# Optimization experiments

Hardware: AMD Instinct MI355X
Metric: run time of the kernel (lower is better)

## Reference

```python
import jax, jax.numpy as jnp
import numpy as np

N_V, N_Q, K, C, FF, OUT, H = 100000, 20000, 48, 128, 256, 128, 8
EPS = 1e-5

def _bn(x, g, b):
    # BatchNorm1d in training mode: biased batch stats over the voxel dim
    m = jnp.mean(x, axis=0)
    v = jnp.var(x, axis=0)
    return (x - m) * jax.lax.rsqrt(v + EPS) * g + b

def setup_inputs():
    key = jax.random.key(0)
    ks = jax.random.split(key, 12)
    s = 0.05
    return {
        "voxel_features": jax.random.normal(ks[0], (N_V, C), jnp.float32),
        "voxel_coords": jax.random.uniform(ks[1], (N_V, 3), jnp.float32) * 70.0,
        "query_coords": jax.random.uniform(ks[2], (N_Q, 3), jnp.float32) * 70.0,
        "wq3": jax.random.normal(ks[3], (3, C), jnp.float32) * s,
        "bq3": jnp.zeros((C,), jnp.float32),
        "wk3": jax.random.normal(ks[4], (3, C), jnp.float32) * s,
        "bk3": jnp.zeros((C,), jnp.float32),
        "in_proj_w": jax.random.normal(ks[5], (3 * C, C), jnp.float32) * s,
        "in_proj_b": jnp.zeros((3 * C,), jnp.float32),
        "out_w": jax.random.normal(ks[6], (C, C), jnp.float32) * s,
        "out_b": jnp.zeros((C,), jnp.float32),
        "w1": jax.random.normal(ks[7], (C, FF), jnp.float32) * s,
        "b1": jnp.zeros((FF,), jnp.float32),
        "w2": jax.random.normal(ks[8], (FF, C), jnp.float32) * s,
        "b2": jnp.zeros((C,), jnp.float32),
        "g1": jnp.ones((C,), jnp.float32),
        "be1": jnp.zeros((C,), jnp.float32),
        "w_out": jax.random.normal(ks[9], (C, OUT), jnp.float32) * s,
        "b_out": jnp.zeros((OUT,), jnp.float32),
        "g2": jnp.ones((OUT,), jnp.float32),
        "be2": jnp.zeros((OUT,), jnp.float32),
        "key_indices": jax.random.randint(ks[10], (N_Q, K), 0, N_V, dtype=jnp.int32),
        "key_mask": (jax.random.randint(ks[11], (N_Q, K), 0, 2) == 1).at[:, 0].set(False),
    }

def reference(voxel_features, voxel_coords, query_coords, wq3, bq3, wk3, bk3,
              in_proj_w, in_proj_b, out_w, out_b, w1, b1, w2, b2, g1, be1,
              w_out, b_out, g2, be2, key_indices, key_mask):
    Dh = C // H
    scale = 1.0 / np.sqrt(Dh)
    # ---- hash-based neighbor gather (grouping_operation) ----
    key_feat = voxel_features[key_indices]                                 # (Nq, K, C)
    key_c = voxel_coords[key_indices] - query_coords[:, None, :]           # relative coords (Nq, K, 3)
    key_feat = key_feat + jax.nn.relu(key_c @ wk3 + bk3)                   # k_pos_proj (Conv1d k=1)
    q_feat = jax.nn.relu(query_coords @ wq3 + bq3)[:, None, :]             # q_pos_proj (Nq, 1, C)
    # ---- multi-head attention: each query attends over its K gathered keys ----
    wq, wk, wv = jnp.split(in_proj_w, 3, axis=0)
    bq_, bk_, bv_ = jnp.split(in_proj_b, 3)
    q = ((q_feat @ wq.T + bq_) * scale).reshape(N_Q, 1, H, Dh)
    k = (key_feat @ wk.T + bk_).reshape(N_Q, K, H, Dh)
    v = (key_feat @ wv.T + bv_).reshape(N_Q, K, H, Dh)
    scores = jnp.einsum('nqhd,nkhd->nhqk', q, k)                           # (Nq, H, 1, K)
    scores = jnp.where(key_mask[:, None, None, :], -1e9, scores)
    attn = jax.nn.softmax(scores, axis=-1)
    o = jnp.einsum('nhqk,nkhd->nqhd', attn, v).reshape(N_Q, 1, C)
    x = (o @ out_w.T + out_b)[:, 0]                                        # (Nq, C)
    # ---- FFN residual + BatchNorm + output head (dropout = eval identity) ----
    x = x + (jax.nn.relu(x @ w1 + b1) @ w2 + b2)
    x = _bn(x, g1, be1)
    y = jax.nn.relu(_bn(x @ w_out + b_out, g2, be2))
    return y
```

## Files before the change

kernel.cpp:

```cpp
#include <hip/hip_runtime.h>
#include <stdint.h>

#define KNN 48
#define CH  128

__device__ __forceinline__ float bf2f(unsigned short u){
  union { unsigned int i; float f; } v; v.i = ((unsigned int)u) << 16; return v.f;
}
__device__ __forceinline__ unsigned short f2bf(float f){
  union { float f; unsigned int i; } v; v.f = f;
  unsigned int x = v.i;
  x += 0x7fffu + ((x >> 16) & 1u);
  return (unsigned short)(x >> 16);
}
template<int MODE>
__device__ __forceinline__ float ld1(const void* p, size_t i){
  if (MODE) return ((const float*)p)[i];
  return bf2f(((const unsigned short*)p)[i]);
}
template<int MODE>
__device__ __forceinline__ void vload4(float* o, const void* p, size_t i){
  if (MODE){
    float4 v = *(const float4*)((const float*)p + i);
    o[0] = v.x; o[1] = v.y; o[2] = v.z; o[3] = v.w;
  } else {
    uint2 v = *(const uint2*)((const unsigned short*)p + i);
    union { unsigned int u; float f; } a, b, c, d;
    a.u = v.x << 16; b.u = v.x & 0xFFFF0000u;
    c.u = v.y << 16; d.u = v.y & 0xFFFF0000u;
    o[0] = a.f; o[1] = b.f; o[2] = c.f; o[3] = d.f;
  }
}
__device__ __forceinline__ void lds_bf4(float* o, const unsigned short* p){
  uint2 v = *(const uint2*)p;
  union { unsigned int u; float f; } a, b, c, d;
  a.u = v.x << 16; b.u = v.x & 0xFFFF0000u;
  c.u = v.y << 16; d.u = v.y & 0xFFFF0000u;
  o[0] = a.f; o[1] = b.f; o[2] = c.f; o[3] = d.f;
}
__device__ __forceinline__ void sts_bf4(unsigned short* p, const float* v){
  unsigned int lo = (unsigned int)f2bf(v[0]) | ((unsigned int)f2bf(v[1]) << 16);
  unsigned int hi = (unsigned int)f2bf(v[2]) | ((unsigned int)f2bf(v[3]) << 16);
  uint2 w; w.x = lo; w.y = hi;
  *(uint2*)p = w;
}

__global__ __launch_bounds__(256) void detect_k(const void* qc, const void* kmask, int* hdr){
  __shared__ int cnt, flg;
  int t = threadIdx.x;
  if (t == 0){ cnt = 0; flg = 0; }
  __syncthreads();
  float v = bf2f(((const unsigned short*)qc)[t]);
  if (v >= 0.f && v <= 70.5f) atomicAdd(&cnt, 1);
  const unsigned int* mw = (const unsigned int*)kmask;
  int f = 0;
  for (int i = t; i < 384; i += 256){
    unsigned int w = mw[i];
    if (w != 0u && w != 1u) f |= 1;
    if (w != 0u && w != 0x3F800000u) f |= 2;
    if (w == 0x3F800000u) f |= 4;
    unsigned int lo = w & 0xFFFFu, hi = w >> 16;
    if ((lo != 0u && lo != 0x3F80u) || (hi != 0u && hi != 0x3F80u)) f |= 8;
    if (lo == 0x3F80u || hi == 0x3F80u) f |= 16;
  }
  if (f) atomicOr(&flg, f);
  __syncthreads();
  if (t == 0){
    int F = flg;
    hdr[0] = (cnt >= 240) ? 0 : 1;
    int fmt;
    if (!(F & 2) && (F & 4)) fmt = 3;
    else if (!(F & 8) && (F & 16)) fmt = 2;
    else if (!(F & 1)) fmt = 0;
    else fmt = 1;
    hdr[1] = fmt;
  }
}

template<int MODE>
__device__ void attn_body(char* pool,
  const void* vf, const void* vc, const void* qc,
  const void* wq3, const void* bq3, const void* wk3, const void* bk3,
  const void* ipw, const void* ipb,
  const int* kidx, const void* kmask,
  unsigned short* O, int fmt)
{
  unsigned short* kf2 = (unsigned short*)(pool);
  float* qfv8 = (float*)(pool);
  float* qkl2 = (float*)(pool + 26112);
  float* sa2  = (float*)(pool + 34560);
  float* qv8  = (float*)(pool + 37888);
  float* wk3s = (float*)(pool + 42112);
  float* bk3s = (float*)(pool + 43648);
  float* sb8  = (float*)(pool + 44160);
  float* rel2 = (float*)(pool + 44416);
  float* mb2  = (float*)(pool + 45568);
  int*   idxs2= (int*)  (pool + 45952);
  float* rden2= (float*)(pool + 46336);
  float* qc8  = (float*)(pool + 46400);

  int t = threadIdx.x;
  int qbase = blockIdx.x * 8;

  for (int i = t; i < 384; i += 256) wk3s[i] = ld1<MODE>(wk3, i);
  if (t < 128) bk3s[t] = ld1<MODE>(bk3, t);
  if (t < 24)  qc8[t]  = ld1<MODE>(qc, (size_t)qbase * 3 + t);
  __syncthreads();

  if (t < 128){
    float w0 = ld1<MODE>(wq3, t), w1 = ld1<MODE>(wq3, 128 + t);
    float w2 = ld1<MODE>(wq3, 256 + t), bb = ld1<MODE>(bq3, t);
    for (int q = 0; q < 8; ++q){
      float a = qc8[q * 3 + 0] * w0 + qc8[q * 3 + 1] * w1 + qc8[q * 3 + 2] * w2 + bb;
      qfv8[q * 132 + t] = fmaxf(a, 0.f);
    }
  }
  __syncthreads();

  {
    int j = t & 127, qg = (t >> 7) * 4;
    float a0 = 0.f, a1 = 0.f, a2 = 0.f, a3 = 0.f;
    for (int c = 0; c < 128; c += 4){
      float w[4];
      vload4<MODE>(w, ipw, (size_t)j * CH + c);
      for (int u = 0; u < 4; ++u){
        float wv = w[u];
        a0 += qfv8[(qg + 0) * 132 + c + u] * wv;
        a1 += qfv8[(qg + 1) * 132 + c + u] * wv;
        a2 += qfv8[(qg + 2) * 132 + c + u] * wv;
        a3 += qfv8[(qg + 3) * 132 + c + u] * wv;
      }
    }
    float bb = ld1<MODE>(ipb, j);
    qv8[(qg + 0) * 132 + j] = (a0 + bb) * 0.25f;
    qv8[(qg + 1) * 132 + j] = (a1 + bb) * 0.25f;
    qv8[(qg + 2) * 132 + j] = (a2 + bb) * 0.25f;
    qv8[(qg + 3) * 132 + j] = (a3 + bb) * 0.25f;
  }
  __syncthreads();

  if (t < 64){
    int q = t >> 3, h = t & 7;
    float sb = 0.f;
    for (int d = 0; d < 16; ++d) sb += qv8[q * 132 + h * 16 + d] * ld1<MODE>(ipb, 128 + h * 16 + d);
    sb8[t] = sb;
  }

  for (int p = 0; p < 4; ++p){
    __syncthreads();

    if (t < 96){
      int q = t / 48, kk = t - q * 48;
      int n = qbase + 2 * p + q;
      int iv = kidx[(size_t)n * KNN + kk];
      idxs2[q * 48 + kk] = iv;
      rel2[q * 144 + kk * 3 + 0] = ld1<MODE>(vc, (size_t)iv * 3 + 0) - qc8[(2 * p + q) * 3 + 0];
      rel2[q * 144 + kk * 3 + 1] = ld1<MODE>(vc, (size_t)iv * 3 + 1) - qc8[(2 * p + q) * 3 + 1];
      rel2[q * 144 + kk * 3 + 2] = ld1<MODE>(vc, (size_t)iv * 3 + 2) - qc8[(2 * p + q) * 3 + 2];
      int mi = n * KNN + kk;
      int mval;
      if (fmt == 0)      mval = (((const int*)kmask)[mi] != 0);
      else if (fmt == 1) mval = (((const unsigned char*)kmask)[mi] != 0);
      else if (fmt == 2) mval = (((const unsigned short*)kmask)[mi] != 0);
      else               mval = (((const unsigned int*)kmask)[mi] != 0);
      mb2[q * 48 + kk] = mval ? -1e9f : 0.f;
    }
    __syncthreads();

    for (int it = 0; it < 12; ++it){
      int q = it / 6;
      int idx4 = (it - q * 6) * 1024 + t * 4;
      int k = idx4 >> 7, c = idx4 & 127;
      int iv = idxs2[q * 48 + k];
      float v[4];
      vload4<MODE>(v, vf, (size_t)iv * CH + c);
      float r0 = rel2[q * 144 + k * 3 + 0], r1 = rel2[q * 144 + k * 3 + 1], r2 = rel2[q * 144 + k * 3 + 2];
      float o[4];
      for (int u = 0; u < 4; ++u){
        float pe = fmaxf(r0 * wk3s[c + u] + r1 * wk3s[128 + c + u] + r2 * wk3s[256 + c + u] + bk3s[c + u], 0.f);
        o[u] = v[u] + pe;
      }
      sts_bf4(kf2 + q * 6528 + k * 136 + c, o);
    }
    {
      int h = t >> 5, cb = (t & 31) << 2;
      float aa0 = 0.f, aa1 = 0.f, aa2 = 0.f, aa3 = 0.f;
      float ab0 = 0.f, ab1 = 0.f, ab2 = 0.f, ab3 = 0.f;
      int qla = (2 * p) * 132 + h * 16, qlb = (2 * p + 1) * 132 + h * 16;
      for (int d = 0; d < 16; ++d){
        float w[4];
        vload4<MODE>(w, ipw, (size_t)(128 + h * 16 + d) * CH + cb);
        float qa = qv8[qla + d], qb = qv8[qlb + d];
        aa0 += qa * w[0]; aa1 += qa * w[1]; aa2 += qa * w[2]; aa3 += qa * w[3];
        ab0 += qb * w[0]; ab1 += qb * w[1]; ab2 += qb * w[2]; ab3 += qb * w[3];
      }
      qkl2[h * 132 + cb + 0] = aa0; qkl2[h * 132 + cb + 1] = aa1;
      qkl2[h * 132 + cb + 2] = aa2; qkl2[h * 132 + cb + 3] = aa3;
      qkl2[1056 + h * 132 + cb + 0] = ab0; qkl2[1056 + h * 132 + cb + 1] = ab1;
      qkl2[1056 + h * 132 + cb + 2] = ab2; qkl2[1056 + h * 132 + cb + 3] = ab3;
    }
    __syncthreads();

    for (int pp = 0; pp < 3; ++pp){
      int did = pp * 256 + t;
      int q = (did >= 384) ? 1 : 0;
      int r = did - q * 384;
      int h = r & 7, k = r >> 3;
      const unsigned short* kr = kf2 + q * 6528 + k * 136;
      const float* qr = qkl2 + q * 1056 + h * 132;
      float acc = 0.f;
      for (int c = 0; c < 128; c += 4){
        float kv[4];
        lds_bf4(kv, kr + c);
        acc += qr[c + 0] * kv[0] + qr[c + 1] * kv[1] + qr[c + 2] * kv[2] + qr[c + 3] * kv[3];
      }
      sa2[q * 416 + h * 52 + k] = acc + sb8[(2 * p + q) * 8 + h] + mb2[q * 48 + k];
    }
    __syncthreads();

    if (t < 16){
      int q = t >> 3, h = t & 7;
      float* s = sa2 + q * 416 + h * 52;
      float m = -1e30f;
      for (int k = 0; k < KNN; ++k) m = fmaxf(m, s[k]);
      float den = 0.f;
      for (int k = 0; k < KNN; ++k){ float e = __expf(s[k] - m); s[k] = e; den += e; }
      rden2[t] = 1.f / den;
    }
    __syncthreads();

    for (int q = 0; q < 2; ++q){
      int h = t & 7, cb = (t >> 3) << 2;
      const float* s = sa2 + q * 416 + h * 52;
      const unsigned short* kb = kf2 + q * 6528;
      float a0 = 0.f, a1 = 0.f, a2 = 0.f, a3 = 0.f;
      for (int k = 0; k < KNN; ++k){
        float av = s[k];
        float kv[4];
        lds_bf4(kv, kb + k * 136 + cb);
        a0 += av * kv[0]; a1 += av * kv[1]; a2 += av * kv[2]; a3 += av * kv[3];
      }
      float rd = rden2[q * 8 + h];
      qkl2[q * 1056 + h * 132 + cb + 0] = a0 * rd;
      qkl2[q * 1056 + h * 132 + cb + 1] = a1 * rd;
      qkl2[q * 1056 + h * 132 + cb + 2] = a2 * rd;
      qkl2[q * 1056 + h * 132 + cb + 3] = a3 * rd;
    }
    __syncthreads();

    {
      int j = t & 127, half = t >> 7, h = j >> 4;
      float acca = 0.f, accb = 0.f;
      int c0 = half * 64;
      for (int c = c0; c < c0 + 64; c += 4){
        float w[4];
        vload4<MODE>(w, ipw, (size_t)(256 + j) * CH + c);
        acca += qkl2[h * 132 + c + 0] * w[0] + qkl2[h * 132 + c + 1] * w[1]
              + qkl2[h * 132 + c + 2] * w[2] + qkl2[h * 132 + c + 3] * w[3];
        accb += qkl2[1056 + h * 132 + c + 0] * w[0] + qkl2[1056 + h * 132 + c + 1] * w[1]
              + qkl2[1056 + h * 132 + c + 2] * w[2] + qkl2[1056 + h * 132 + c + 3] * w[3];
      }
      sa2[half * 128 + j] = acca;
      sa2[512 + half * 128 + j] = accb;
    }
    __syncthreads();

    {
      int q = t >> 7, j = t & 127;
      float o = sa2[q * 512 + j] + sa2[q * 512 + 128 + j] + ld1<MODE>(ipb, 256 + j);
      O[(size_t)(qbase + 2 * p + q) * CH + j] = f2bf(o);
    }
  }
}

__global__ __launch_bounds__(256, 3) void attn_k(
  const void* vf, const void* vc, const void* qc,
  const void* wq3, const void* bq3, const void* wk3, const void* bk3,
  const void* ipw, const void* ipb,
  const int* kidx, const void* kmask,
  unsigned short* O, const int* hdr)
{
  __shared__ __attribute__((aligned(16))) char pool[46496];
  int mode = hdr[0], fmt = hdr[1];
  if (mode) attn_body<1>(pool, vf, vc, qc, wq3, bq3, wk3, bk3, ipw, ipb, kidx, kmask, O, fmt);
  else      attn_body<0>(pool, vf, vc, qc, wq3, bq3, wk3, bk3, ipw, ipb, kidx, kmask, O, fmt);
}

template<int MODE>
__device__ void opffn_body(char* pool, const unsigned short* SRC, unsigned short* DST,
    const void* outw, const void* outb, const void* w1, const void* b1,
    const void* w2, const void* b2, float* stats1)
{
  float* Os = (float*)pool;
  unsigned short* Ws = (unsigned short*)(pool + 16384);
  unsigned short* Hs = (unsigned short*)(pool + 16384);
  float* ssum = (float*)(pool + 32768);
  float* ssq  = (float*)(pool + 33280);
  int tid = threadIdx.x;
  int mbase = blockIdx.x * 32;

  for (int i = 0; i < 4; ++i){
    int idx4 = (tid + i * 256) * 4;
    int r = idx4 >> 7, c = idx4 & 127;
    lds_bf4(Os + idx4, SRC + (size_t)(mbase + r) * 128 + c);
  }
  for (int i = 0; i < 16; ++i){
    int q = tid + i * 256;
    int j = q >> 5, c4 = (q & 31) * 4;
    float w[4];
    vload4<MODE>(w, outw, (size_t)j * 128 + c4);
    Ws[(c4 + 0) * 129 + j] = f2bf(w[0]);
    Ws[(c4 + 1) * 129 + j] = f2bf(w[1]);
    Ws[(c4 + 2) * 129 + j] = f2bf(w[2]);
    Ws[(c4 + 3) * 129 + j] = f2bf(w[3]);
  }
  __syncthreads();

  int j = tid & 127, rh = tid >> 7;
  float acc[16];
  for (int r = 0; r < 16; ++r) acc[r] = 0.f;
  for (int c = 0; c < 128; ++c){
    float wv = bf2f(Ws[c * 129 + j]);
    for (int r = 0; r < 16; ++r) acc[r] += Os[(rh * 16 + r) * 128 + c] * wv;
  }
  float bbo = ld1<MODE>(outb, j);
  __syncthreads();
  for (int r = 0; r < 16; ++r) Os[(rh * 16 + r) * 128 + j] = acc[r] + bbo;
  __syncthreads();

  {
    if (tid < 128){ ssum[tid] = 0.f; ssq[tid] = 0.f; }
    float a[32];
    for (int r = 0; r < 32; ++r) a[r] = 0.f;
    for (int c = 0; c < 128; ++c){
      float wv = ld1<MODE>(w1, (size_t)c * 256 + tid);
      for (int r = 0; r < 32; ++r) a[r] += Os[r * 128 + c] * wv;
    }
    float bb1 = ld1<MODE>(b1, tid);
    for (int r = 0; r < 32; ++r) Hs[r * 256 + tid] = f2bf(fmaxf(a[r] + bb1, 0.f));
  }
  __syncthreads();

  int col = tid & 127;
  float a2[16];
  for (int r = 0; r < 16; ++r) a2[r] = 0.f;
  for (int jj = 0; jj < 256; ++jj){
    float wv = ld1<MODE>(w2, (size_t)jj * 128 + col);
    for (int r = 0; r < 16; ++r) a2[r] += bf2f(Hs[(rh * 16 + r) * 256 + jj]) * wv;
  }
  float bb2 = ld1<MODE>(b2, col);
  float ls = 0.f, lq = 0.f;
  for (int r = 0; r < 16; ++r){
    float x = a2[r] + bb2 + Os[(rh * 16 + r) * 128 + col];
    DST[(size_t)(mbase + rh * 16 + r) * 128 + col] = f2bf(x);
    ls += x; lq += x * x;
  }
  atomicAdd(&ssum[col], ls);
  atomicAdd(&ssq[col], lq);
  __syncthreads();
  if (tid < 128){
    float* bank = stats1 + (size_t)(blockIdx.x & 7) * 256;
    atomicAdd(bank + tid, ssum[tid]);
    atomicAdd(bank + 128 + tid, ssq[tid]);
  }
}

__global__ __launch_bounds__(256) void opffn_k(const unsigned short* SRC, unsigned short* DST,
    const void* outw, const void* outb, const void* w1, const void* b1,
    const void* w2, const void* b2, float* stats1, const int* hdr)
{
  __shared__ __attribute__((aligned(16))) char pool[49408];
  if (hdr[0]) opffn_body<1>(pool, SRC, DST, outw, outb, w1, b1, w2, b2, stats1);
  else        opffn_body<0>(pool, SRC, DST, outw, outb, w1, b1, w2, b2, stats1);
}

template<int MODE>
__device__ void head_body(char* pool, unsigned short* AD, const float* stats1,
    const void* g1, const void* be1, const void* wout, const void* bout, float* stats2)
{
  float* s1 = (float*)pool;
  float* t1 = (float*)(pool + 512);
  float* Xs = (float*)(pool + 1024);
  float* ssum = (float*)(pool + 17408);
  float* ssq  = (float*)(pool + 17920);
  int tid = threadIdx.x;
  int mbase = blockIdx.x * 32;
  if (tid < 128){
    float s = 0.f, sq = 0.f;
    for (int b = 0; b < 8; ++b){ s += stats1[b * 256 + tid]; sq += stats1[b * 256 + 128 + tid]; }
    float m = s * (1.f / 20000.f);
    float var = sq * (1.f / 20000.f) - m * m;
    float sc = ld1<MODE>(g1, tid) * rsqrtf(var + 1e-5f);
    s1[tid] = sc;
    t1[tid] = ld1<MODE>(be1, tid) - m * sc;
    ssum[tid] = 0.f; ssq[tid] = 0.f;
  }
  __syncthreads();
  for (int i = 0; i < 4; ++i){
    int idx4 = (tid + i * 256) * 4;
    int r = idx4 >> 7, c = idx4 & 127;
    float v[4];
    lds_bf4(v, AD + (size_t)(mbase + r) * 128 + c);
    Xs[idx4 + 0] = s1[c + 0] * v[0] + t1[c + 0];
    Xs[idx4 + 1] = s1[c + 1] * v[1] + t1[c + 1];
    Xs[idx4 + 2] = s1[c + 2] * v[2] + t1[c + 2];
    Xs[idx4 + 3] = s1[c + 3] * v[3] + t1[c + 3];
  }
  __syncthreads();
  int tcol = tid & 127, rh = tid >> 7;
  float acc[16];
  for (int r = 0; r < 16; ++r) acc[r] = 0.f;
  for (int k = 0; k < 128; ++k){
    float wv = ld1<MODE>(wout, (size_t)k * 128 + tcol);
    for (int r = 0; r < 16; ++r) acc[r] += Xs[(rh * 16 + r) * 128 + k] * wv;
  }
  float bb = ld1<MODE>(bout, tcol);
  float ls = 0.f, lq = 0.f;
  for (int r = 0; r < 16; ++r){
    float z = acc[r] + bb;
    AD[(size_t)(mbase + rh * 16 + r) * 128 + tcol] = f2bf(z);
    ls += z; lq += z * z;
  }
  atomicAdd(&ssum[tcol], ls);
  atomicAdd(&ssq[tcol], lq);
  __syncthreads();
  if (tid < 128){
    float* bank = stats2 + (size_t)(blockIdx.x & 7) * 256;
    atomicAdd(bank + tid, ssum[tid]);
    atomicAdd(bank + 128 + tid, ssq[tid]);
  }
}

__global__ __launch_bounds__(256) void head_k(unsigned short* AD, const float* stats1,
    const void* g1, const void* be1, const void* wout, const void* bout,
    float* stats2, const int* hdr)
{
  __shared__ __attribute__((aligned(16))) char pool[18432];
  if (hdr[0]) head_body<1>(pool, AD, stats1, g1, be1, wout, bout, stats2);
  else        head_body<0>(pool, AD, stats1, g1, be1, wout, bout, stats2);
}

template<int MODE>
__device__ void bn2_body(float* ss, float* tt, const unsigned short* Z, void* out,
    const float* S2, const void* g2, const void* be2)
{
  int t = threadIdx.x;
  if (t < 128){
    float s = 0.f, sq = 0.f;
    for (int b = 0; b < 8; ++b){ s += S2[b * 256 + t]; sq += S2[b * 256 + 128 + t]; }
    float m = s * (1.f / 20000.f);
    float var = sq * (1.f / 20000.f) - m * m;
    float sc = ld1<MODE>(g2, t) * rsqrtf(var + 1e-5f);
    ss[t] = sc;
    tt[t] = ld1<MODE>(be2, t) - m * sc;
  }
  __syncthreads();
  size_t base = ((size_t)blockIdx.x * 256 + t) * 4;
  int c = (int)(base & 127);
  float v[4];
  lds_bf4(v, Z + base);
  float y0 = fmaxf(v[0] * ss[c + 0] + tt[c + 0], 0.f);
  float y1 = fmaxf(v[1] * ss[c + 1] + tt[c + 1], 0.f);
  float y2 = fmaxf(v[2] * ss[c + 2] + tt[c + 2], 0.f);
  float y3 = fmaxf(v[3] * ss[c + 3] + tt[c + 3], 0.f);
  if (MODE){
    float4 o; o.x = y0; o.y = y1; o.z = y2; o.w = y3;
    *(float4*)((float*)out + base) = o;
  } else {
    float yv[4] = {y0, y1, y2, y3};
    sts_bf4((unsigned short*)out + base, yv);
  }
}

__global__ __launch_bounds__(256) void bn2_k(const unsigned short* Z, void* out,
    const float* S2, const void* g2, const void* be2, const int* hdr)
{
  __shared__ float ss[128], tt[128];
  if (hdr[0]) bn2_body<1>(ss, tt, Z, out, S2, g2, be2);
  else        bn2_body<0>(ss, tt, Z, out, S2, g2, be2);
}

extern "C" void kernel_launch(void* const* d_in, const int* in_sizes, int n_in,
                              void* d_out, int out_size, void* d_ws, size_t ws_size,
                              hipStream_t stream)
{
  const void* vf    = d_in[0];
  const void* vc    = d_in[1];
  const void* qcrd  = d_in[2];
  const void* wq3   = d_in[3];
  const void* bq3   = d_in[4];
  const void* wk3   = d_in[5];
  const void* bk3   = d_in[6];
  const void* ipw   = d_in[7];
  const void* ipb   = d_in[8];
  const void* out_w = d_in[9];
  const void* out_b = d_in[10];
  const void* w1    = d_in[11];
  const void* b1    = d_in[12];
  const void* w2    = d_in[13];
  const void* b2    = d_in[14];
  const void* g1    = d_in[15];
  const void* be1   = d_in[16];
  const void* wout2 = d_in[17];
  const void* bout2 = d_in[18];
  const void* g2    = d_in[19];
  const void* be2   = d_in[20];
  const int*  kidx  = (const int*)d_in[21];
  const void* kmask = d_in[22];

  char* ws = (char*)d_ws;
  int*   hdr    = (int*)(ws + 0);
  float* stats1 = (float*)(ws + 1024);
  float* stats2 = (float*)(ws + 9216);

  unsigned short* O     = (unsigned short*)d_out;
  unsigned short* arena = (unsigned short*)d_in[0];

  hipMemsetAsync(ws, 0, 17408, stream);
  detect_k<<<1, 256, 0, stream>>>(qcrd, kmask, hdr);
  attn_k<<<2500, 256, 0, stream>>>(vf, vc, qcrd, wq3, bq3, wk3, bk3, ipw, ipb, kidx, kmask, O, hdr);
  opffn_k<<<625, 256, 0, stream>>>(O, arena, out_w, out_b, w1, b1, w2, b2, stats1, hdr);
  head_k<<<625, 256, 0, stream>>>(arena, stats1, g1, be1, wout2, bout2, stats2, hdr);
  bn2_k<<<2500, 256, 0, stream>>>(arena, d_out, stats2, g2, be2, hdr);
}
```

Measured before the change: 593.7 us.

## Use bf16 MFMA with hi/lo split for attention score and value products

Replaces the scalar LDS dot products for the query-key scores and the attention-weighted key sum with 16x16x32 bf16 MFMA instructions. The fp32 operands (projected query, attention weights) are split into hi and lo bf16 parts so the products keep near-fp32 precision, at the cost of twice the MFMA count. The aim is to cut VALU and LDS-read cost in the inner attention loops. Shared memory grows from about 46 KB to about 53 KB, which may lower occupancy below the requested 3 blocks per CU. There is also an odd 0.5 scaling on keys 16-31 that looks like a workaround for the padded second K tile, which could affect correctness.

```diff
diff --git a/kernel.cpp b/kernel.cpp
--- a/kernel.cpp
+++ b/kernel.cpp
@@ -3,6 +3,9 @@
 
 #define KNN 48
 #define CH  128
+
+typedef __attribute__((ext_vector_type(8))) short bf16x8;
+typedef __attribute__((ext_vector_type(4))) float f32x4;
 
 __device__ __forceinline__ float bf2f(unsigned short u){
   union { unsigned int i; float f; } v; v.i = ((unsigned int)u) << 16; return v.f;
@@ -87,17 +90,21 @@
 {
   unsigned short* kf2 = (unsigned short*)(pool);
   float* qfv8 = (float*)(pool);
-  float* qkl2 = (float*)(pool + 26112);
-  float* sa2  = (float*)(pool + 34560);
-  float* qv8  = (float*)(pool + 37888);
-  float* wk3s = (float*)(pool + 42112);
-  float* bk3s = (float*)(pool + 43648);
-  float* sb8  = (float*)(pool + 44160);
-  float* rel2 = (float*)(pool + 44416);
-  float* mb2  = (float*)(pool + 45568);
-  int*   idxs2= (int*)  (pool + 45952);
-  float* rden2= (float*)(pool + 46336);
-  float* qc8  = (float*)(pool + 46400);
+  unsigned short* qkhi = (unsigned short*)(pool + 26112);
+  unsigned short* qklo = (unsigned short*)(pool + 30464);
+  float* af   = (float*)(pool + 26112);
+  float* sa2  = (float*)(pool + 34816);
+  float* qv8  = (float*)(pool + 38144);
+  float* wk3s = (float*)(pool + 42368);
+  float* bk3s = (float*)(pool + 43904);
+  float* sb8  = (float*)(pool + 44416);
+  float* rel2 = (float*)(pool + 44672);
+  float* mb2  = (float*)(pool + 45824);
+  int*   idxs2= (int*)  (pool + 46208);
+  float* rden2= (float*)(pool + 46592);
+  float* qc8  = (float*)(pool + 46656);
+  unsigned short* athi = (unsigned short*)(pool + 46752);
+  unsigned short* atlo = (unsigned short*)(pool + 49824);
 
   int t = threadIdx.x;
   int qbase = blockIdx.x * 8;
@@ -194,27 +201,49 @@
         aa0 += qa * w[0]; aa1 += qa * w[1]; aa2 += qa * w[2]; aa3 += qa * w[3];
         ab0 += qb * w[0]; ab1 += qb * w[1]; ab2 += qb * w[2]; ab3 += qb * w[3];
       }
-      qkl2[h * 132 + cb + 0] = aa0; qkl2[h * 132 + cb + 1] = aa1;
-      qkl2[h * 132 + cb + 2] = aa2; qkl2[h * 132 + cb + 3] = aa3;
-      qkl2[1056 + h * 132 + cb + 0] = ab0; qkl2[1056 + h * 132 + cb + 1] = ab1;
-      qkl2[1056 + h * 132 + cb + 2] = ab2; qkl2[1056 + h * 132 + cb + 3] = ab3;
-    }
-    __syncthreads();
-
-    for (int pp = 0; pp < 3; ++pp){
-      int did = pp * 256 + t;
-      int q = (did >= 384) ? 1 : 0;
-      int r = did - q * 384;
-      int h = r & 7, k = r >> 3;
-      const unsigned short* kr = kf2 + q * 6528 + k * 136;
-      const float* qr = qkl2 + q * 1056 + h * 132;
-      float acc = 0.f;
-      for (int c = 0; c < 128; c += 4){
-        float kv[4];
-        lds_bf4(kv, kr + c);
-        acc += qr[c + 0] * kv[0] + qr[c + 1] * kv[1] + qr[c + 2] * kv[2] + qr[c + 3] * kv[3];
+      unsigned short h0 = f2bf(aa0), h1 = f2bf(aa1), h2 = f2bf(aa2), h3 = f2bf(aa3);
+      uint2 w0; w0.x = (unsigned)h0 | ((unsigned)h1 << 16); w0.y = (unsigned)h2 | ((unsigned)h3 << 16);
+      *(uint2*)(qkhi + h * 136 + cb) = w0;
+      unsigned short e0 = f2bf(aa0 - bf2f(h0)), e1 = f2bf(aa1 - bf2f(h1));
+      unsigned short e2 = f2bf(aa2 - bf2f(h2)), e3 = f2bf(aa3 - bf2f(h3));
+      uint2 w1; w1.x = (unsigned)e0 | ((unsigned)e1 << 16); w1.y = (unsigned)e2 | ((unsigned)e3 << 16);
+      *(uint2*)(qklo + h * 136 + cb) = w1;
+      unsigned short g0 = f2bf(ab0), g1 = f2bf(ab1), g2 = f2bf(ab2), g3 = f2bf(ab3);
+      uint2 w2; w2.x = (unsigned)g0 | ((unsigned)g1 << 16); w2.y = (unsigned)g2 | ((unsigned)g3 << 16);
+      *(uint2*)(qkhi + 1088 + h * 136 + cb) = w2;
+      unsigned short f0 = f2bf(ab0 - bf2f(g0)), f1 = f2bf(ab1 - bf2f(g1));
+      unsigned short f2 = f2bf(ab2 - bf2f(g2)), f3 = f2bf(ab3 - bf2f(g3));
+      uint2 w3; w3.x = (unsigned)f0 | ((unsigned)f1 << 16); w3.y = (unsigned)f2 | ((unsigned)f3 << 16);
+      *(uint2*)(qklo + 1088 + h * 136 + cb) = w3;
+    }
+    __syncthreads();
+
+    {
+      int w = t >> 6, lane = t & 63, g = lane >> 4, cc = lane & 15;
+      int q = w >> 1;
+      int t0 = (w & 1) ? 2 : 0, t1 = (w & 1) ? 3 : 2;
+      const unsigned short* qh = qkhi + q * 1088 + cc * 136;
+      const unsigned short* ql = qklo + q * 1088 + cc * 136;
+      for (int tile = t0; tile < t1; ++tile){
+        const unsigned short* kb = kf2 + q * 6528 + (tile * 16 + cc) * 136 + g * 8;
+        f32x4 acc = {0.f, 0.f, 0.f, 0.f};
+        #pragma unroll
+        for (int kk = 0; kk < 4; ++kk){
+          bf16x8 ah = *(const bf16x8*)(qh + kk * 32 + g * 8);
+          bf16x8 al = *(const bf16x8*)(ql + kk * 32 + g * 8);
+          bf16x8 bb = *(const bf16x8*)(kb + kk * 32);
+          acc = __builtin_amdgcn_mfma_f32_16x16x32_bf16(ah, bb, acc, 0, 0, 0);
+          acc = __builtin_amdgcn_mfma_f32_16x16x32_bf16(al, bb, acc, 0, 0, 0);
+        }
+        if (lane < 32){
+          int key = tile * 16 + cc;
+          #pragma unroll
+          for (int r = 0; r < 4; ++r){
+            int h = g * 4 + r;
+            sa2[q * 416 + h * 52 + key] = acc[r] + sb8[(2 * p + q) * 8 + h] + mb2[q * 48 + key];
+          }
+        }
       }
-      sa2[q * 416 + h * 52 + k] = acc + sb8[(2 * p + q) * 8 + h] + mb2[q * 48 + k];
     }
     __syncthreads();
 
@@ -229,22 +258,53 @@
     }
     __syncthreads();
 
-    for (int q = 0; q < 2; ++q){
-      int h = t & 7, cb = (t >> 3) << 2;
-      const float* s = sa2 + q * 416 + h * 52;
-      const unsigned short* kb = kf2 + q * 6528;
-      float a0 = 0.f, a1 = 0.f, a2 = 0.f, a3 = 0.f;
-      for (int k = 0; k < KNN; ++k){
-        float av = s[k];
-        float kv[4];
-        lds_bf4(kv, kb + k * 136 + cb);
-        a0 += av * kv[0]; a1 += av * kv[1]; a2 += av * kv[2]; a3 += av * kv[3];
+    #pragma unroll
+    for (int u = 0; u < 3; ++u){
+      int id = t + 256 * u;
+      int q = id >= 384;
+      int r = id - q * 384;
+      int h = (r * 683) >> 15;
+      int k = r - h * 48;
+      float a = sa2[q * 416 + h * 52 + k] * rden2[q * 8 + h];
+      if (k >= 16 && k < 32) a *= 0.5f;
+      unsigned short hi = f2bf(a);
+      athi[(q * 16 + h) * 48 + k] = hi;
+      atlo[(q * 16 + h) * 48 + k] = f2bf(a - bf2f(hi));
+    }
+    __syncthreads();
+
+    {
+      int w = t >> 6, lane = t & 63, g = lane >> 4, cc = lane & 15;
+      int q = w >> 1;
+      int T0 = (w & 1) * 4;
+      const unsigned short* A0 = athi + q * 768 + cc * 48;
+      const unsigned short* A1 = atlo + q * 768 + cc * 48;
+      bf16x8 a1h = *(const bf16x8*)(A0 + g * 8);
+      bf16x8 a1l = *(const bf16x8*)(A1 + g * 8);
+      bf16x8 a2h = *(const bf16x8*)(A0 + 16 + g * 8);
+      bf16x8 a2l = *(const bf16x8*)(A1 + 16 + g * 8);
+      const unsigned short* kq = kf2 + q * 6528;
+      for (int T = 0; T < 4; ++T){
+        int c = (T0 + T) * 16 + cc;
+        bf16x8 b1, b2;
+        #pragma unroll
+        for (int j = 0; j < 8; ++j){
+          b1[j] = (short)kq[(g * 8 + j) * 136 + c];
+          b2[j] = (short)kq[(16 + g * 8 + j) * 136 + c];
+        }
+        f32x4 acc = {0.f, 0.f, 0.f, 0.f};
+        acc = __builtin_amdgcn_mfma_f32_16x16x32_bf16(a1h, b1, acc, 0, 0, 0);
+        acc = __builtin_amdgcn_mfma_f32_16x16x32_bf16(a1l, b1, acc, 0, 0, 0);
+        acc = __builtin_amdgcn_mfma_f32_16x16x32_bf16(a2h, b2, acc, 0, 0, 0);
+        acc = __builtin_amdgcn_mfma_f32_16x16x32_bf16(a2l, b2, acc, 0, 0, 0);
+        if (lane < 32){
+          #pragma unroll
+          for (int r = 0; r < 4; ++r){
+            int h = g * 4 + r;
+            af[q * 1056 + h * 132 + c] = acc[r];
+          }
+        }
       }
-      float rd = rden2[q * 8 + h];
-      qkl2[q * 1056 + h * 132 + cb + 0] = a0 * rd;
-      qkl2[q * 1056 + h * 132 + cb + 1] = a1 * rd;
-      qkl2[q * 1056 + h * 132 + cb + 2] = a2 * rd;
-      qkl2[q * 1056 + h * 132 + cb + 3] = a3 * rd;
     }
     __syncthreads();
 
@@ -255,10 +315,10 @@
       for (int c = c0; c < c0 + 64; c += 4){
         float w[4];
         vload4<MODE>(w, ipw, (size_t)(256 + j) * CH + c);
-        acca += qkl2[h * 132 + c + 0] * w[0] + qkl2[h * 132 + c + 1] * w[1]
-              + qkl2[h * 132 + c + 2] * w[2] + qkl2[h * 132 + c + 3] * w[3];
-        accb += qkl2[1056 + h * 132 + c + 0] * w[0] + qkl2[1056 + h * 132 + c + 1] * w[1]
-              + qkl2[1056 + h * 132 + c + 2] * w[2] + qkl2[1056 + h * 132 + c + 3] * w[3];
+        acca += af[h * 132 + c + 0] * w[0] + af[h * 132 + c + 1] * w[1]
+              + af[h * 132 + c + 2] * w[2] + af[h * 132 + c + 3] * w[3];
+        accb += af[1056 + h * 132 + c + 0] * w[0] + af[1056 + h * 132 + c + 1] * w[1]
+              + af[1056 + h * 132 + c + 2] * w[2] + af[1056 + h * 132 + c + 3] * w[3];
       }
       sa2[half * 128 + j] = acca;
       sa2[512 + half * 128 + j] = accb;
@@ -280,7 +340,7 @@
   const int* kidx, const void* kmask,
   unsigned short* O, const int* hdr)
 {
-  __shared__ __attribute__((aligned(16))) char pool[46496];
+  __shared__ __attribute__((aligned(16))) char pool[52896];
   int mode = hdr[0], fmt = hdr[1];
   if (mode) attn_body<1>(pool, vf, vc, qc, wq3, bq3, wk3, bk3, ipw, ipb, kidx, kmask, O, fmt);
   else      attn_body<0>(pool, vf, vc, qc, wq3, bq3, wk3, bk3, ipw, ipb, kidx, kmask, O, fmt);
```

Result: slower. 622.6 us (+4.9%).
